# Optimization experiments

Hardware: AMD Instinct MI355X
Metric: run time of the kernel (lower is better)

Reference implementation:

```python
import jax, jax.numpy as jnp
import numpy as np

EPS_NORM = 1e-12  # F.normalize eps
EPS_BN = 1e-5     # BatchNorm2d eps


def _neighbor_idx(h, w):
    # Replicates get_window_mask's clamped 3x3 neighbor indices (hw, 9).
    off = np.array([-1, 0, 1])
    x_off = np.tile(off, 3)        # [-1,0,1,-1,0,1,-1,0,1]
    y_off = np.repeat(off, 3)      # [-1,-1,-1,0,0,0,1,1,1]
    yy, xx = np.meshgrid(np.arange(h), np.arange(w), indexing='ij')
    x_nn = np.clip(xx.reshape(-1, 1) + x_off[None, :], 0, w - 1)
    y_nn = np.clip(yy.reshape(-1, 1) + y_off[None, :], 0, h - 1)
    return jnp.asarray(y_nn * w + x_nn, dtype=jnp.int32)  # (hw, 9)


def _find_nn(xf, yf, idx):
    # Faithful to find_nn: cosine sim between cur pixel and 3x3 window of y,
    # argmin over the (masked-in) window, gather the NORMALIZED y feature.
    # The dense (hw,hw) matmul + 9999 mask reduces exactly to these 9 candidates.
    b, c, h, w = xf.shape
    xn = xf.reshape(b, c, h * w).transpose(0, 2, 1)  # (b, hw, c)
    xn = xn / jnp.maximum(jnp.linalg.norm(xn, axis=-1, keepdims=True), EPS_NORM)
    yn = yf.reshape(b, c, h * w)
    yn = yn / jnp.maximum(jnp.linalg.norm(yn, axis=1, keepdims=True), EPS_NORM)
    ynt = yn.transpose(0, 2, 1)          # (b, hw, c)
    y_nb = ynt[:, idx, :]                # (b, hw, 9, c) gathered neighbors
    sims = jnp.einsum('bpc,bpkc->bpk', xn, y_nb)  # (b, hw, 9)
    k = jnp.argmin(sims, axis=-1)
    nnv = jnp.take_along_axis(y_nb, k[:, :, None, None], axis=2)[:, :, 0, :]
    return nnv.transpose(0, 2, 1).reshape(b, c, h, w)


def _forward(x, conv_w, bn_gamma, bn_beta):
    h, w = x.shape[-2:]
    prev_f, next_f, cur_f = x[:, 0], x[:, 1], x[:, 2]
    idx = _neighbor_idx(h, w)
    nn_prev = _find_nn(cur_f, prev_f, idx)
    nn_next = _find_nn(cur_f, next_f, idx)
    feat = jnp.concatenate([nn_prev, nn_next, cur_f], axis=1)  # (b, 3c, h, w)
    out = jnp.einsum('oc,bchw->bohw', conv_w, feat)            # 1x1 conv, no bias
    # BatchNorm2d in training mode: per-channel batch stats (biased var)
    mean = out.mean(axis=(0, 2, 3), keepdims=True)
    var = out.var(axis=(0, 2, 3), keepdims=True)
    out = (out - mean) * jax.lax.rsqrt(var + EPS_BN)
    out = out * bn_gamma[None, :, None, None] + bn_beta[None, :, None, None]
    out = jax.nn.relu(out)
    return jnp.stack([prev_f, next_f, out], axis=1)  # (b, 3, c, h, w)


def setup_inputs() -> dict:
    key = jax.random.key(0)
    k1, k2 = jax.random.split(key)
    b, c, h, w = 8, 256, 64, 64
    x = jax.random.normal(k1, (b, 3, c, h, w), dtype=jnp.float32)
    fan_in, fan_out = 3 * c, c
    bound = float(np.sqrt(6.0 / (fan_in + fan_out)))  # xavier_uniform
    conv_w = jax.random.uniform(k2, (c, 3 * c), dtype=jnp.float32, minval=-bound, maxval=bound)
    bn_gamma = jnp.ones((c,), dtype=jnp.float32)
    bn_beta = jnp.zeros((c,), dtype=jnp.float32)
    return {'x': x, 'conv_w': conv_w, 'bn_gamma': bn_gamma, 'bn_beta': bn_beta}


def reference(x, conv_w, bn_gamma, bn_beta):
    return _forward(x, conv_w, bn_gamma, bn_beta)
```

## Files before the change

### kernel.cpp

```cpp
#include <hip/hip_runtime.h>

constexpr int B  = 8;
constexpr int C  = 256;
constexpr int Hh = 64;
constexpr int Ww = 64;
constexpr int P  = Hh * Ww;
constexpr int CP = C * P;
constexpr int CT = 3 * C;
constexpr int J  = B * P;

constexpr int DOT_D_OFF = 0;
constexpr int SSQ_D_OFF = 294912;
constexpr int SEL_F_OFF = 663552;
constexpr int SIV_F_OFF = 671744;
constexpr int WB_F_OFF  = 679936;

typedef __attribute__((ext_vector_type(8))) short short8;
typedef __attribute__((ext_vector_type(4))) float f32x4;

__device__ inline unsigned short bf16_rne(float f) {
    unsigned u = __float_as_uint(f);
    return (unsigned short)((u + 0x7fffu + ((u >> 16) & 1u)) >> 16);
}
__device__ inline unsigned pack2(float a, float b) {
    return (unsigned)bf16_rne(a) | ((unsigned)bf16_rne(b) << 16);
}

__global__ __launch_bounds__(256) void k_wcvt(const float* __restrict__ Wg,
                                              unsigned short* __restrict__ Wb) {
    int i = blockIdx.x * 256 + threadIdx.x;
    Wb[i] = bf16_rne(Wg[i]);
}

__global__ __launch_bounds__(256) void k_dots(const float* __restrict__ x,
                                              float* __restrict__ out) {
    __shared__ float ys[2][2][2][6][64];
    __shared__ float cs[2][2][256];
    const int t     = threadIdx.x;
    const int b     = blockIdx.x >> 4;
    const int strip = blockIdx.x & 15;
    const int chunk = blockIdx.y;
    const int y0 = strip * 4;
    const int ry = t >> 6;
    const int xc = t & 63;
    const int xm = max(xc - 1, 0), xp = min(xc + 1, 63);
    const int c0 = chunk * 64;

    size_t gbase;
    float *d00, *d01, *d10, *d11;
    float* ysf = &ys[0][0][0][0][0];
    float* csf = &cs[0][0][0];
    if (t < 64) {
        gbase = (size_t)(b * 3 + 2) * CP + (size_t)c0 * P + strip * 256 + t * 4;
        int l0 = t * 4;
        d00 = csf + l0;        d01 = csf + 256 + l0;
        d10 = csf + 512 + l0;  d11 = csf + 768 + l0;
    } else {
        int i   = t - 64;
        int sid = i >= 96;
        int r   = (i - sid * 96) >> 4;
        int x4  = i & 15;
        int yl  = min(max(y0 - 1 + r, 0), Hh - 1);
        gbase = (size_t)(b * 3 + sid) * CP + (size_t)c0 * P + yl * 64 + x4 * 4;
        int l0 = (sid * 6 + r) * 64 + x4 * 4;
        d00 = ysf + l0;         d01 = ysf + 768 + l0;
        d10 = ysf + 1536 + l0;  d11 = ysf + 1536 + 768 + l0;
    }

    double d[2][9] = {{0,0,0,0,0,0,0,0,0},{0,0,0,0,0,0,0,0,0}};
    double qs[2] = {0.0, 0.0};

    f32x4 a0 = *(const f32x4*)(x + gbase);
    f32x4 a1 = *(const f32x4*)(x + gbase + (size_t)P);
    f32x4 b0 = *(const f32x4*)(x + gbase + (size_t)2 * P);
    f32x4 b1 = *(const f32x4*)(x + gbase + (size_t)3 * P);

    #define COMPUTE(BUF, CH)                                                 \
    {                                                                        \
        double cd = (double)cs[BUF][CH][t];                                  \
        _Pragma("unroll")                                                    \
        for (int s = 0; s < 2; ++s) {                                        \
            const float* Y0 = &ys[BUF][CH][s][ry][0];         \
            const float* Y1 = Y0 + 64;                        \
            const float* Y2 = Y1 + 64;                        \
            d[s][0] = fma(cd, (double)Y0[xm], d[s][0]);                      \
            d[s][1] = fma(cd, (double)Y0[xc], d[s][1]);                      \
            d[s][2] = fma(cd, (double)Y0[xp], d[s][2]);                      \
            d[s][3] = fma(cd, (double)Y1[xm], d[s][3]);                      \
            d[s][4] = fma(cd, (double)Y1[xc], d[s][4]);                      \
            d[s][5] = fma(cd, (double)Y1[xp], d[s][5]);                      \
            d[s][6] = fma(cd, (double)Y2[xm], d[s][6]);                      \
            d[s][7] = fma(cd, (double)Y2[xc], d[s][7]);                      \
            d[s][8] = fma(cd, (double)Y2[xp], d[s][8]);                      \
            double ov = (double)Y1[xc];                                      \
            qs[s] = fma(ov, ov, qs[s]);                                      \
        }                                                                    \
    }

    for (int n = 0; n < 64; n += 4) {
        *(f32x4*)d00 = a0; *(f32x4*)d01 = a1;
        __syncthreads();
        if (n + 4 < 64) {
            a0 = *(const f32x4*)(x + gbase + (size_t)(n + 4) * P);
            a1 = *(const f32x4*)(x + gbase + (size_t)(n + 5) * P);
        }
        COMPUTE(0, 0) COMPUTE(0, 1)
        *(f32x4*)d10 = b0; *(f32x4*)d11 = b1;
        __syncthreads();
        if (n + 6 < 64) {
            b0 = *(const f32x4*)(x + gbase + (size_t)(n + 6) * P);
            b1 = *(const f32x4*)(x + gbase + (size_t)(n + 7) * P);
        }
        COMPUTE(1, 0) COMPUTE(1, 1)
    }
    #undef COMPUTE

    const int p = strip * 256 + t;
    double* db = (double*)(out + (size_t)(b * 3) * CP);
    #pragma unroll
    for (int s = 0; s < 2; ++s) {
        #pragma unroll
        for (int k = 0; k < 9; ++k)
            db[DOT_D_OFF + (size_t)((chunk * 2 + s) * 9 + k) * 4096 + p] = d[s][k];
        db[SSQ_D_OFF + (size_t)(chunk * 2 + s) * 4096 + p] = qs[s];
    }
}

__global__ __launch_bounds__(256) void k_sel(float* __restrict__ out) {
    int gid  = blockIdx.x * 256 + threadIdx.x;
    int side = gid >> 15;
    int j    = gid & (J - 1);
    int b = j >> 12, p = j & (P - 1);
    int y = p >> 6, xc = p & 63;

    int nidx[9];
    #pragma unroll
    for (int k = 0; k < 9; ++k) {
        int dy = k / 3 - 1, dx = k % 3 - 1;
        int yy = min(max(y + dy, 0), Hh - 1);
        int xx = min(max(xc + dx, 0), Ww - 1);
        nidx[k] = yy * Ww + xx;
    }

    const double* db = (const double*)(out + (size_t)(b * 3) * CP) + DOT_D_OFF;
    const double* sb = (const double*)(out + (size_t)(b * 3) * CP) + SSQ_D_OFF;

    double best = 0.0; int bi = 0; float sivbest = 0.0f;
    #pragma unroll
    for (int k = 0; k < 9; ++k) {
        int nq = nidx[k];
        double ssum = ((sb[(0 * 2 + side) * 4096 + nq]
                      + sb[(1 * 2 + side) * 4096 + nq])
                      + sb[(2 * 2 + side) * 4096 + nq])
                      + sb[(3 * 2 + side) * 4096 + nq];
        float ivf = 1.0f / fmaxf((float)sqrt(ssum), 1e-12f);
        double sk = ((db[(size_t)((0 * 2 + side) * 9 + k) * 4096 + p]
                    + db[(size_t)((1 * 2 + side) * 9 + k) * 4096 + p])
                    + db[(size_t)((2 * 2 + side) * 9 + k) * 4096 + p])
                    + db[(size_t)((3 * 2 + side) * 9 + k) * 4096 + p];
        double s = sk * (double)ivf;
        if (k == 0 || s < best) { best = s; bi = k; sivbest = ivf; }
    }
    int*   selb = (int*)(out + (size_t)(b * 3) * CP + SEL_F_OFF);
    float* sivb = out + (size_t)(b * 3) * CP + SIV_F_OFF;
    selb[side * 4096 + p] = nidx[bi];
    sivb[side * 4096 + p] = sivbest;
}

__global__ __launch_bounds__(512) void k_gemm(const float* __restrict__ x,
                                              const unsigned short* __restrict__ Wb,
                                              float* __restrict__ out) {
    __shared__ unsigned short As[2][4][256][8];
    __shared__ unsigned short Bs[2][4][128][8];
    __shared__ int   sel_s[2][128];
    __shared__ float siv_s[2][128];

    const int t  = threadIdx.x;
    const int j0 = blockIdx.x * 128;
    const int b  = j0 >> 12, p0 = j0 & (P - 1);

    if (t < 256) {
        int side = t >> 7, jj = t & 127;
        const int*   selb = (const int*)(out + (size_t)(b * 3) * CP + SEL_F_OFF);
        const float* sivb = out + (size_t)(b * 3) * CP + SIV_F_OFF;
        sel_s[side][jj] = selb[side * 4096 + p0 + jj];
        siv_s[side][jj] = sivb[side * 4096 + p0 + jj];
    }
    __syncthreads();

    const int lane = t & 63, w = t >> 6;
    const int q = lane >> 4, l16 = lane & 15;
    const int m0w = (w & 3) * 64;
    const int n0w = (w >> 2) * 64;

    const int jj = t & 127, kq = (t >> 7) & 3;
    const int ma = t & 255, kh = t >> 8;
    const int k0 = kq * 8;

    const float* pp = x + (size_t)(b * 3 + 0) * CP + sel_s[0][jj];
    const float* np = x + (size_t)(b * 3 + 1) * CP + sel_s[1][jj];
    const float* cp = x + (size_t)(b * 3 + 2) * CP + p0 + jj;
    const float  sp = siv_s[0][jj], sn = siv_s[1][jj];
    const unsigned short* wbase = Wb + (size_t)ma * CT + kh * 16;

    f32x4 acc[4][4];
    #pragma unroll
    for (int f = 0; f < 4; ++f)
        #pragma unroll
        for (int g = 0; g < 4; ++g)
            acc[f][g] = (f32x4){0.f, 0.f, 0.f, 0.f};

    short8 wa0, wa1;
    float fb[8];
    float scale;

    #define LOAD_STEP(KK)                                                    \
    {                                                                        \
        const unsigned short* wsrc = wbase + (KK);                           \
        wa0 = *(const short8*)wsrc;                                          \
        wa1 = *(const short8*)(wsrc + 8);                                    \
        const float* src;                                                    \
        if ((KK) < 256)      { src = pp + (size_t)((KK) + k0) * P;       scale = sp;   } \
        else if ((KK) < 512) { src = np + (size_t)((KK) - 256 + k0) * P; scale = sn;   } \
        else                 { src = cp + (size_t)((KK) - 512 + k0) * P; scale = 1.0f; } \
        _Pragma("unroll")                                                    \
        for (int u = 0; u < 8; ++u) fb[u] = src[(size_t)u * P];              \
    }

    #define WRITE_STEP(BUF)                                                  \
    {                                                                        \
        *(short8*)&As[BUF][kh * 2    ][ma][0] = wa0;                         \
        *(short8*)&As[BUF][kh * 2 + 1][ma][0] = wa1;                         \
        uint4 pk = make_uint4(pack2(fb[0] * scale, fb[1] * scale),           \
                              pack2(fb[2] * scale, fb[3] * scale),           \
                              pack2(fb[4] * scale, fb[5] * scale),           \
                              pack2(fb[6] * scale, fb[7] * scale));          \
        *(uint4*)&Bs[BUF][kq][jj][0] = pk;                                   \
    }

    LOAD_STEP(0)
    WRITE_STEP(0)
    __syncthreads();

    for (int i = 0; i < 24; ++i) {
        if (i + 1 < 24) LOAD_STEP((i + 1) * 32)
        const int cur = i & 1;
        short8 af[4], bfr[4];
        #pragma unroll
        for (int f = 0; f < 4; ++f)
            af[f] = *(const short8*)&As[cur][q][m0w + f * 16 + l16][0];
        #pragma unroll
        for (int g = 0; g < 4; ++g)
            bfr[g] = *(const short8*)&Bs[cur][q][n0w + g * 16 + l16][0];
        #pragma unroll
        for (int f = 0; f < 4; ++f)
            #pragma unroll
            for (int g = 0; g < 4; ++g)
                acc[f][g] = __builtin_amdgcn_mfma_f32_16x16x32_bf16(
                    af[f], bfr[g], acc[f][g], 0, 0, 0);
        if (i + 1 < 24) WRITE_STEP((i + 1) & 1)
        __syncthreads();
    }
    #undef LOAD_STEP
    #undef WRITE_STEP

    float* outb = out + (size_t)(b * 3 + 2) * CP;
    #pragma unroll
    for (int f = 0; f < 4; ++f)
        #pragma unroll
        for (int g = 0; g < 4; ++g)
            #pragma unroll
            for (int r = 0; r < 4; ++r) {
                int ch  = m0w + f * 16 + q * 4 + r;
                int col = p0 + n0w + g * 16 + l16;
                outb[(size_t)ch * P + col] = acc[f][g][r];
            }
}

__global__ __launch_bounds__(256) void k_bn(float* __restrict__ out,
                                            const float* __restrict__ gamma,
                                            const float* __restrict__ beta) {
    __shared__ double rs[256], rq[256];
    __shared__ float sc_s, sh_s;
    const int o = blockIdx.x, t = threadIdx.x;

    double s = 0.0, q = 0.0;
    for (int b = 0; b < B; ++b) {
        const float4* base =
            (const float4*)(out + (size_t)(b * 3 + 2) * CP + (size_t)o * P);
        #pragma unroll
        for (int i = 0; i < 4; ++i) {
            float4 v = base[i * 256 + t];
            s += (double)v.x + (double)v.y + (double)v.z + (double)v.w;
            q += (double)v.x * v.x + (double)v.y * v.y
               + (double)v.z * v.z + (double)v.w * v.w;
        }
    }
    rs[t] = s; rq[t] = q;
    __syncthreads();
    for (int off = 128; off > 0; off >>= 1) {
        if (t < off) { rs[t] += rs[t + off]; rq[t] += rq[t + off]; }
        __syncthreads();
    }
    if (t == 0) {
        double mean = rs[0] * (1.0 / (double)J);
        double var  = rq[0] * (1.0 / (double)J) - mean * mean;
        double inv  = 1.0 / sqrt(var + 1e-5);
        double sc   = (double)gamma[o] * inv;
        sc_s = (float)sc;
        sh_s = (float)((double)beta[o] - mean * sc);
    }
    __syncthreads();
    const float sc = sc_s, sh = sh_s;

    for (int b = 0; b < B; ++b) {
        float4* base =
            (float4*)(out + (size_t)(b * 3 + 2) * CP + (size_t)o * P);
        #pragma unroll
        for (int i = 0; i < 4; ++i) {
            float4 v = base[i * 256 + t];
            v.x = fmaxf(fmaf(v.x, sc, sh), 0.f);
            v.y = fmaxf(fmaf(v.y, sc, sh), 0.f);
            v.z = fmaxf(fmaf(v.z, sc, sh), 0.f);
            v.w = fmaxf(fmaf(v.w, sc, sh), 0.f);
            base[i * 256 + t] = v;
        }
    }
}

__global__ __launch_bounds__(256) void k_copy(const float4* __restrict__ x4,
                                              float4* __restrict__ o4) {
    int tid = blockIdx.x * blockDim.x + threadIdx.x;
    const int per_b = 2 * CP / 4;
    const int bstr  = 3 * CP / 4;
    if (tid < B * per_b) {
        int b = tid / per_b;
        int r = tid - b * per_b;
        o4[b * bstr + r] = x4[b * bstr + r];
    }
}

extern "C" void kernel_launch(void* const* d_in, const int* in_sizes, int n_in,
                              void* d_out, int out_size, void* d_ws, size_t ws_size,
                              hipStream_t stream) {
    const float* x     = (const float*)d_in[0];
    const float* wconv = (const float*)d_in[1];
    const float* gamma = (const float*)d_in[2];
    const float* beta  = (const float*)d_in[3];
    float* out = (float*)d_out;
    (void)d_ws; (void)ws_size;

    unsigned short* Wbuf = (unsigned short*)(out + WB_F_OFF);

    k_wcvt<<<CT * C / 256, 256, 0, stream>>>(wconv, Wbuf);

    k_dots<<<dim3(128, 4), 256, 0, stream>>>(x, out);

    k_sel<<<2 * J / 256, 256, 0, stream>>>(out);

    k_gemm<<<J / 128, 512, 0, stream>>>(x, Wbuf, out);

    k_bn<<<C, 256, 0, stream>>>(out, gamma, beta);

    k_copy<<<(B * 2 * CP / 4 + 255) / 256, 256, 0, stream>>>(
        (const float4*)x, (float4*)out);
}
```

Measured before the change: 262.0 us.

## Fuse BatchNorm statistics into GEMM epilogue via double atomics

The GEMM epilogue now reduces per-channel sum and sum of squares from its accumulators, first with warp shuffles, then through shared memory, and adds them into a global double buffer with atomicAdd. The BN kernel then reads those statistics and makes a single normalize-and-ReLU pass instead of first re-reading the whole conv output to compute them. The statistics buffer is zeroed in the weight-conversion kernel. Partial sums are now formed in float before the double atomics, which costs some precision, and the GEMM epilogue gains a barrier and extra atomic traffic.

After: 257.3 us. Within noise of the previous version (-1.8%).

```diff
diff --git a/kernel.cpp b/kernel.cpp
--- a/kernel.cpp
+++ b/kernel.cpp
@@ -14,6 +14,7 @@
 constexpr int SEL_F_OFF = 663552;
 constexpr int SIV_F_OFF = 671744;
 constexpr int WB_F_OFF  = 679936;
+constexpr int BNS_D_OFF = 389120;
 
 typedef __attribute__((ext_vector_type(8))) short short8;
 typedef __attribute__((ext_vector_type(4))) float f32x4;
@@ -27,9 +28,15 @@
 }
 
 __global__ __launch_bounds__(256) void k_wcvt(const float* __restrict__ Wg,
-                                              unsigned short* __restrict__ Wb) {
+                                              unsigned short* __restrict__ Wb,
+                                              float* __restrict__ out) {
     int i = blockIdx.x * 256 + threadIdx.x;
     Wb[i] = bf16_rne(Wg[i]);
+    if (blockIdx.x == 0) {
+        double* bns = (double*)out + BNS_D_OFF;
+        bns[threadIdx.x]       = 0.0;
+        bns[256 + threadIdx.x] = 0.0;
+    }
 }
 
 __global__ __launch_bounds__(256) void k_dots(const float* __restrict__ x,
@@ -174,6 +181,7 @@
     __shared__ unsigned short Bs[2][4][128][8];
     __shared__ int   sel_s[2][128];
     __shared__ float siv_s[2][128];
+    __shared__ float sw_s[8][64], sw_q[8][64];
 
     const int t  = threadIdx.x;
     const int j0 = blockIdx.x * 128;
@@ -275,43 +283,46 @@
                 int col = p0 + n0w + g * 16 + l16;
                 outb[(size_t)ch * P + col] = acc[f][g][r];
             }
+
+    #pragma unroll
+    for (int f = 0; f < 4; ++f)
+        #pragma unroll
+        for (int r = 0; r < 4; ++r) {
+            float s  = acc[f][0][r] + acc[f][1][r] + acc[f][2][r] + acc[f][3][r];
+            float qq = acc[f][0][r] * acc[f][0][r] + acc[f][1][r] * acc[f][1][r]
+                     + acc[f][2][r] * acc[f][2][r] + acc[f][3][r] * acc[f][3][r];
+            #pragma unroll
+            for (int m = 1; m <= 8; m <<= 1) {
+                s  += __shfl_xor(s, m);
+                qq += __shfl_xor(qq, m);
+            }
+            if (l16 == 0) {
+                sw_s[w][f * 16 + q * 4 + r] = s;
+                sw_q[w][f * 16 + q * 4 + r] = qq;
+            }
+        }
+    __syncthreads();
+    if (t < 256) {
+        int quad = t >> 6, lch = t & 63;
+        double s  = (double)sw_s[quad][lch] + (double)sw_s[4 + quad][lch];
+        double qq = (double)sw_q[quad][lch] + (double)sw_q[4 + quad][lch];
+        double* bns = (double*)out + BNS_D_OFF;
+        atomicAdd(&bns[t], s);
+        atomicAdd(&bns[256 + t], qq);
+    }
 }
 
 __global__ __launch_bounds__(256) void k_bn(float* __restrict__ out,
                                             const float* __restrict__ gamma,
                                             const float* __restrict__ beta) {
-    __shared__ double rs[256], rq[256];
-    __shared__ float sc_s, sh_s;
     const int o = blockIdx.x, t = threadIdx.x;
-
-    double s = 0.0, q = 0.0;
-    for (int b = 0; b < B; ++b) {
-        const float4* base =
-            (const float4*)(out + (size_t)(b * 3 + 2) * CP + (size_t)o * P);
-        #pragma unroll
-        for (int i = 0; i < 4; ++i) {
-            float4 v = base[i * 256 + t];
-            s += (double)v.x + (double)v.y + (double)v.z + (double)v.w;
-            q += (double)v.x * v.x + (double)v.y * v.y
-               + (double)v.z * v.z + (double)v.w * v.w;
-        }
-    }
-    rs[t] = s; rq[t] = q;
-    __syncthreads();
-    for (int off = 128; off > 0; off >>= 1) {
-        if (t < off) { rs[t] += rs[t + off]; rq[t] += rq[t + off]; }
-        __syncthreads();
-    }
-    if (t == 0) {
-        double mean = rs[0] * (1.0 / (double)J);
-        double var  = rq[0] * (1.0 / (double)J) - mean * mean;
-        double inv  = 1.0 / sqrt(var + 1e-5);
-        double sc   = (double)gamma[o] * inv;
-        sc_s = (float)sc;
-        sh_s = (float)((double)beta[o] - mean * sc);
-    }
-    __syncthreads();
-    const float sc = sc_s, sh = sh_s;
+    const double* bns = (const double*)out + BNS_D_OFF;
+    double mean = bns[o] * (1.0 / (double)J);
+    double var  = bns[256 + o] * (1.0 / (double)J) - mean * mean;
+    double inv  = 1.0 / sqrt(var + 1e-5);
+    double scd  = (double)gamma[o] * inv;
+    const float sc = (float)scd;
+    const float sh = (float)((double)beta[o] - mean * scd);
 
     for (int b = 0; b < B; ++b) {
         float4* base =
@@ -352,7 +363,7 @@
 
     unsigned short* Wbuf = (unsigned short*)(out + WB_F_OFF);
 
-    k_wcvt<<<CT * C / 256, 256, 0, stream>>>(wconv, Wbuf);
+    k_wcvt<<<CT * C / 256, 256, 0, stream>>>(wconv, Wbuf, out);
 
     k_dots<<<dim3(128, 4), 256, 0, stream>>>(x, out);
 
```
